# Performance work log

Measured on AMD Instinct MI355X. Metric: run time of the kernel, lower is better.

## Reference

```python
import jax, jax.numpy as jnp
import numpy as np

N, E, R, D = 100000, 1600000, 8, 128

def setup_inputs() -> dict:
    key = jax.random.key(0)
    ks = jax.random.split(key, 8)
    x = jax.random.normal(ks[0], (N, D), dtype=jnp.float32)
    src = jax.random.randint(ks[1], (E,), 0, N, dtype=jnp.int32)
    dst = jax.random.randint(ks[2], (E,), 0, N, dtype=jnp.int32)
    etype = jax.random.randint(ks[3], (E,), 0, R, dtype=jnp.int32)
    W_rel = jax.random.normal(ks[4], (R, D, D), dtype=jnp.float32) * 0.05
    loop_w = jax.random.normal(ks[5], (D, D), dtype=jnp.float32) * 0.05
    rel_bias = jnp.zeros((D,), dtype=jnp.float32)
    W1 = jax.random.normal(ks[6], (2 * D, 2 * D), dtype=jnp.float32) * 0.05
    b1 = jnp.zeros((2 * D,), dtype=jnp.float32)
    W2 = jax.random.normal(ks[7], (3 * D, D), dtype=jnp.float32) * 0.05
    b2 = jnp.zeros((D,), dtype=jnp.float32)
    return {"x": x, "src": src, "dst": dst, "etype": etype,
            "W_rel": W_rel, "loop_w": loop_w, "rel_bias": rel_bias,
            "W1": W1, "b1": b1, "W2": W2, "b2": b2}

def reference(x, src, dst, etype, W_rel, loop_w, rel_bias, W1, b1, W2, b2):
    # RelGraphConv (low_mem): aggregate source features per (relation, dst) node,
    # then one matmul per relation: msg[i] = sum_r (sum_{e: etype=r, dst=i} x[src_e]) @ W_r
    seg = etype.astype(jnp.int32) * N + dst.astype(jnp.int32)  # combined (rel, dst) id
    agg = jax.ops.segment_sum(x[src], seg, num_segments=R * N)  # [R*N, D]
    agg = agg.reshape(R, N, D)
    msg = jnp.einsum('rnd,rdo->no', agg, W_rel)  # per-relation transform + sum over relations
    msg = msg + x @ loop_w + rel_bias            # DGL default self_loop + bias
    # concat-MLP update (activation = tanh)
    mid = jnp.tanh(jnp.concatenate([x, msg], axis=1) @ W1 + b1)  # [N, 2D]
    out = jnp.concatenate([x, mid], axis=1) @ W2 + b2            # [N, D]
    return out
```

## Files before the change

### kernel.cpp

```cpp
#include <hip/hip_runtime.h>

#define NN 100000
#define DD 128
#define RR 8
#define NSEG (RR*NN)
#define NB1 782
#define ECAP 2048

typedef unsigned short u16;
typedef __bf16 bf16x8 __attribute__((ext_vector_type(8)));
typedef float f32x4 __attribute__((ext_vector_type(4)));
typedef u16 ushort4e __attribute__((ext_vector_type(4)));
typedef unsigned int uint4e __attribute__((ext_vector_type(4)));

__device__ __forceinline__ u16 f2bf(float f){
    union { float f; unsigned u; } v; v.f = f;
    unsigned r = v.u + 0x7fffu + ((v.u >> 16) & 1u);
    return (u16)(r >> 16);
}
__device__ __forceinline__ float bf2f(u16 h){
    union { unsigned u; float f; } v; v.u = ((unsigned)h) << 16; return v.f;
}
__device__ __forceinline__ float ftanh(float x){
    float e = __expf(2.0f * x);
    return 1.0f - 2.0f / (e + 1.0f);
}
__device__ __forceinline__ bf16x8 ldv(const u16* p){
    return *reinterpret_cast<const bf16x8*>(p);
}
__device__ __forceinline__ void gload_lds16(const void* g, void* l){
    __builtin_amdgcn_global_load_lds(
        (const __attribute__((address_space(1))) void*)g,
        (__attribute__((address_space(3))) void*)l, 16, 0, 0);
}

__global__ void k_cast_x(const float* __restrict__ x, u16* __restrict__ xb, int n){
    int i = (blockIdx.x * 256 + threadIdx.x) * 4;
    if (i >= n) return;
    float4 v = *reinterpret_cast<const float4*>(x + i);
    ushort4 o = make_ushort4(f2bf(v.x), f2bf(v.y), f2bf(v.z), f2bf(v.w));
    *reinterpret_cast<ushort4*>(xb + i) = o;
}

__global__ void k_prep_w(const float* __restrict__ Wrel, const float* __restrict__ loopw,
                         const float* __restrict__ W1, const float* __restrict__ W2,
                         u16* __restrict__ WT, u16* __restrict__ W1t, u16* __restrict__ W2t){
    int tid = blockIdx.x * 256 + threadIdx.x;
    if (tid < 131072) {
        int r = tid >> 14, rem = tid & 16383, d = rem >> 7, o = rem & 127;
        WT[(r * 128 + o) * 128 + d] = f2bf(Wrel[tid]);
    } else if (tid < 147456) {
        int i = tid - 131072, d = i >> 7, o = i & 127;
        WT[(8 * 128 + o) * 128 + d] = f2bf(loopw[i]);
    } else if (tid < 212992) {
        int i = tid - 147456, k = i >> 8, n2 = i & 255;
        W1t[n2 * 256 + k] = f2bf(W1[i]);
    } else {
        int i = tid - 212992, k = i >> 7, n2 = i & 127;
        W2t[n2 * 384 + k] = f2bf(W2[i]);
    }
}

__global__ void k_count(const int* __restrict__ et, const int* __restrict__ dst,
                        int* __restrict__ cnt, int* __restrict__ seg, int E){
    int e = blockIdx.x * 256 + threadIdx.x;
    if (e < E){
        int s = et[e] * NN + dst[e];
        seg[e] = s;
        atomicAdd(&cnt[s], 1);
    }
}

__global__ void k_scan1(const int* __restrict__ cnt, int* __restrict__ Off, int* __restrict__ bsum){
    __shared__ int lds[256];
    int t = threadIdx.x;
    int i0 = blockIdx.x * 1024 + t * 4;
    int c0 = (i0 + 0 < NSEG) ? cnt[i0 + 0] : 0;
    int c1 = (i0 + 1 < NSEG) ? cnt[i0 + 1] : 0;
    int c2 = (i0 + 2 < NSEG) ? cnt[i0 + 2] : 0;
    int c3 = (i0 + 3 < NSEG) ? cnt[i0 + 3] : 0;
    int s = c0 + c1 + c2 + c3;
    lds[t] = s; __syncthreads();
    for (int off = 1; off < 256; off <<= 1){
        int v = (t >= off) ? lds[t - off] : 0;
        __syncthreads();
        lds[t] += v;
        __syncthreads();
    }
    int excl = lds[t] - s;
    if (i0 + 0 < NSEG) Off[i0 + 0] = excl; excl += c0;
    if (i0 + 1 < NSEG) Off[i0 + 1] = excl; excl += c1;
    if (i0 + 2 < NSEG) Off[i0 + 2] = excl; excl += c2;
    if (i0 + 3 < NSEG) Off[i0 + 3] = excl;
    if (t == 255) bsum[blockIdx.x] = lds[255];
}

__global__ void k_scan2(int* __restrict__ bsum){
    __shared__ int lds[1024];
    int t = threadIdx.x;
    int v = (t < NB1) ? bsum[t] : 0;
    lds[t] = v; __syncthreads();
    for (int off = 1; off < 1024; off <<= 1){
        int u = (t >= off) ? lds[t - off] : 0;
        __syncthreads();
        lds[t] += u;
        __syncthreads();
    }
    if (t < NB1) bsum[t] = lds[t] - v;
}

__global__ void k_scan3(int* __restrict__ Off, const int* __restrict__ bsum,
                        int* __restrict__ cursor, int E){
    int base = bsum[blockIdx.x];
    int t = threadIdx.x;
    int i0 = blockIdx.x * 1024 + t * 4;
    #pragma unroll
    for (int j = 0; j < 4; ++j){
        int i = i0 + j;
        if (i < NSEG){ int v = Off[i] + base; Off[i] = v; cursor[i] = v; }
    }
    if (blockIdx.x == 0 && t == 0) Off[NSEG] = E;
}

__global__ void k_scatter(const int* __restrict__ seg, const int* __restrict__ src,
                          int* __restrict__ cursor, int* __restrict__ esrc, int E){
    int e = blockIdx.x * 256 + threadIdx.x;
    if (e < E){
        int pos = atomicAdd(&cursor[seg[e]], 1);
        esrc[pos] = src[e];
    }
}

__global__ __launch_bounds__(256) void k_agg(
    const u16* __restrict__ xb, const int* __restrict__ Off,
    const int* __restrict__ esrc, u16* __restrict__ agg)
{
    __shared__ int offs[33];
    __shared__ int eidx[ECAP];
    const int tid = threadIdx.x;
    const int s0 = blockIdx.x * 32;
    if (tid < 33) offs[tid] = Off[s0 + tid];
    __syncthreads();
    const int base = offs[0];
    const int tot = offs[32] - base;
    const bool inlds = (tot <= ECAP);
    if (inlds){
        for (int i = tid; i < tot; i += 256) eidx[i] = esrc[base + i];
    }
    __syncthreads();

    const int hw = tid >> 5;
    const int lid = tid & 31;
    const int c = lid * 4;

    #pragma unroll
    for (int j = 0; j < 4; ++j){
        const int sj = hw * 4 + j;
        const int lo = offs[sj] - base;
        const int hi = offs[sj + 1] - base;
        float a0 = 0.f, a1 = 0.f, a2 = 0.f, a3 = 0.f;
        int e = lo;
        if (inlds){
            for (; e + 4 <= hi; e += 4){
                int i0 = eidx[e], i1 = eidx[e+1], i2 = eidx[e+2], i3 = eidx[e+3];
                ushort4 v0 = *reinterpret_cast<const ushort4*>(xb + (size_t)i0 * DD + c);
                ushort4 v1 = *reinterpret_cast<const ushort4*>(xb + (size_t)i1 * DD + c);
                ushort4 v2 = *reinterpret_cast<const ushort4*>(xb + (size_t)i2 * DD + c);
                ushort4 v3 = *reinterpret_cast<const ushort4*>(xb + (size_t)i3 * DD + c);
                a0 += bf2f(v0.x) + bf2f(v1.x) + bf2f(v2.x) + bf2f(v3.x);
                a1 += bf2f(v0.y) + bf2f(v1.y) + bf2f(v2.y) + bf2f(v3.y);
                a2 += bf2f(v0.z) + bf2f(v1.z) + bf2f(v2.z) + bf2f(v3.z);
                a3 += bf2f(v0.w) + bf2f(v1.w) + bf2f(v2.w) + bf2f(v3.w);
            }
            for (; e < hi; ++e){
                int i = eidx[e];
                ushort4 v = *reinterpret_cast<const ushort4*>(xb + (size_t)i * DD + c);
                a0 += bf2f(v.x); a1 += bf2f(v.y); a2 += bf2f(v.z); a3 += bf2f(v.w);
            }
        } else {
            for (; e < hi; ++e){
                int i = esrc[base + e];
                ushort4 v = *reinterpret_cast<const ushort4*>(xb + (size_t)i * DD + c);
                a0 += bf2f(v.x); a1 += bf2f(v.y); a2 += bf2f(v.z); a3 += bf2f(v.w);
            }
        }
        ushort4e o;
        o.x = f2bf(a0); o.y = f2bf(a1); o.z = f2bf(a2); o.w = f2bf(a3);
        __builtin_nontemporal_store(o,
            reinterpret_cast<ushort4e*>(agg + (size_t)(s0 + sj) * DD + c));
    }
}

__global__ __launch_bounds__(512) void k_fused(
    const u16* __restrict__ xb, const u16* __restrict__ agg,
    const u16* __restrict__ WT, const u16* __restrict__ W1t, const u16* __restrict__ W2t,
    const float* __restrict__ relb, const float* __restrict__ bb1, const float* __restrict__ bb2,
    float* __restrict__ out)
{
    __shared__ __align__(16) u16 smem[25088];
    u16 (*bufA)[128] = (u16(*)[128])(smem);
    u16 (*bufB)[128] = (u16(*)[128])(smem + 8192);
    u16 (*msgs)[136] = (u16(*)[136])(smem + 16384);
    u16 (*mids)[264] = (u16(*)[264])(smem + 8192);

    const int tid = threadIdx.x;
    const int w = tid >> 6;
    const int lane = tid & 63;
    const int l15 = lane & 15;
    const int l4 = lane >> 4;
    const int kof = l4 * 8;
    const int swz = (l15 & 7) << 3;
    const int b64 = blockIdx.x * 64;

    const int Wb0 = w * 1024 + (lane << 4);
    auto stage_dma = [&](u16* buf, const u16* grows){
        #pragma unroll
        for (int is = 0; is < 2; ++is){
            int W = Wb0 + is * 8192;
            int row = W >> 8;
            int srcrow = (b64 + row < NN) ? row : 0;
            int inrow = (W & 255) ^ ((row & 7) << 4);
            const char* src = (const char*)(grows + (size_t)srcrow * DD) + inrow;
            gload_lds16(src, (char*)buf + W);
        }
    };

    f32x4 acc[4];
    #pragma unroll
    for (int mi = 0; mi < 4; ++mi)
        #pragma unroll
        for (int q = 0; q < 4; ++q) acc[mi][q] = 0.f;

    stage_dma(&bufA[0][0], agg + (size_t)b64 * DD);
    __syncthreads();

    for (int r = 0; r <= 8; ++r){
        if (r < 7)       stage_dma((r & 1) ? &bufA[0][0] : &bufB[0][0],
                                   agg + ((size_t)(r + 1) * NN + b64) * DD);
        else if (r == 7) stage_dma(&bufA[0][0], xb + (size_t)b64 * DD);
        const u16 (*A)[128] = (r & 1) ? bufB : bufA;
        const u16* B = WT + r * (DD * DD);
        #pragma unroll
        for (int kc = 0; kc < 4; ++kc){
            int cA = (kc * 32 + kof) ^ swz;
            bf16x8 a0 = ldv(&A[l15][cA]);
            bf16x8 a1 = ldv(&A[16 + l15][cA]);
            bf16x8 a2 = ldv(&A[32 + l15][cA]);
            bf16x8 a3 = ldv(&A[48 + l15][cA]);
            bf16x8 wv = ldv(B + (w * 16 + l15) * DD + kc * 32 + kof);
            acc[0] = __builtin_amdgcn_mfma_f32_16x16x32_bf16(a0, wv, acc[0], 0, 0, 0);
            acc[1] = __builtin_amdgcn_mfma_f32_16x16x32_bf16(a1, wv, acc[1], 0, 0, 0);
            acc[2] = __builtin_amdgcn_mfma_f32_16x16x32_bf16(a2, wv, acc[2], 0, 0, 0);
            acc[3] = __builtin_amdgcn_mfma_f32_16x16x32_bf16(a3, wv, acc[3], 0, 0, 0);
        }
        __syncthreads();
    }

    {
        int col = w * 16 + l15;
        float bv = relb[col];
        #pragma unroll
        for (int mi = 0; mi < 4; ++mi)
            #pragma unroll
            for (int q = 0; q < 4; ++q)
                msgs[mi * 16 + l4 * 4 + q][col] = f2bf(acc[mi][q] + bv);
    }
    __syncthreads();

    f32x4 acc2[4][2];
    #pragma unroll
    for (int mi = 0; mi < 4; ++mi)
        #pragma unroll
        for (int nj = 0; nj < 2; ++nj)
            #pragma unroll
            for (int q = 0; q < 4; ++q) acc2[mi][nj][q] = 0.f;

    #pragma unroll
    for (int kc = 0; kc < 8; ++kc){
        bf16x8 a[4];
        #pragma unroll
        for (int mi = 0; mi < 4; ++mi)
            a[mi] = (kc < 4) ? ldv(&bufA[mi * 16 + l15][(kc * 32 + kof) ^ swz])
                             : ldv(&msgs[mi * 16 + l15][(kc - 4) * 32 + kof]);
        #pragma unroll
        for (int nj = 0; nj < 2; ++nj){
            int n2 = w * 32 + nj * 16 + l15;
            bf16x8 wv = ldv(W1t + n2 * 256 + kc * 32 + kof);
            #pragma unroll
            for (int mi = 0; mi < 4; ++mi)
                acc2[mi][nj] = __builtin_amdgcn_mfma_f32_16x16x32_bf16(a[mi], wv, acc2[mi][nj], 0, 0, 0);
        }
    }
    __syncthreads();
    #pragma unroll
    for (int nj = 0; nj < 2; ++nj){
        int col = w * 32 + nj * 16 + l15;
        float bv = bb1[col];
        #pragma unroll
        for (int mi = 0; mi < 4; ++mi)
            #pragma unroll
            for (int q = 0; q < 4; ++q)
                mids[mi * 16 + l4 * 4 + q][col] = f2bf(ftanh(acc2[mi][nj][q] + bv));
    }
    __syncthreads();

    f32x4 acc3[4];
    #pragma unroll
    for (int mi = 0; mi < 4; ++mi)
        #pragma unroll
        for (int q = 0; q < 4; ++q) acc3[mi][q] = 0.f;

    #pragma unroll
    for (int kc = 0; kc < 12; ++kc){
        bf16x8 a[4];
        #pragma unroll
        for (int mi = 0; mi < 4; ++mi)
            a[mi] = (kc < 4) ? ldv(&bufA[mi * 16 + l15][(kc * 32 + kof) ^ swz])
                             : ldv(&mids[mi * 16 + l15][(kc - 4) * 32 + kof]);
        bf16x8 wv = ldv(W2t + (w * 16 + l15) * 384 + kc * 32 + kof);
        #pragma unroll
        for (int mi = 0; mi < 4; ++mi)
            acc3[mi] = __builtin_amdgcn_mfma_f32_16x16x32_bf16(a[mi], wv, acc3[mi], 0, 0, 0);
    }

    {
        int col = w * 16 + l15;
        float bv = bb2[col];
        #pragma unroll
        for (int mi = 0; mi < 4; ++mi)
            #pragma unroll
            for (int q = 0; q < 4; ++q){
                int row = b64 + mi * 16 + l4 * 4 + q;
                if (row < NN)
                    __builtin_nontemporal_store(acc3[mi][q] + bv,
                        &out[(size_t)row * DD + col]);
            }
    }
}

extern "C" void kernel_launch(void* const* d_in, const int* in_sizes, int n_in,
                              void* d_out, int out_size, void* d_ws, size_t ws_size,
                              hipStream_t stream){
    const float* x    = (const float*)d_in[0];
    const int*   src  = (const int*)d_in[1];
    const int*   dst  = (const int*)d_in[2];
    const int*   et   = (const int*)d_in[3];
    const float* Wrel = (const float*)d_in[4];
    const float* loopw= (const float*)d_in[5];
    const float* relb = (const float*)d_in[6];
    const float* W1   = (const float*)d_in[7];
    const float* b1   = (const float*)d_in[8];
    const float* W2   = (const float*)d_in[9];
    const float* b2   = (const float*)d_in[10];
    const int E = in_sizes[1];
    float* out = (float*)d_out;

    char* ws = (char*)d_ws;
    u16* xb   = (u16*)(ws);
    u16* WT   = (u16*)(ws + 25600000);
    u16* W1t  = (u16*)(ws + 25894912);
    u16* W2t  = (u16*)(ws + 26025984);
    int* cnt  = (int*)(ws + 26124288);
    int* Off  = (int*)(ws + 29324288);
    int* bsum = (int*)(ws + 32524544);
    int* esrc = (int*)(ws + 32528640);
    u16* agg  = (u16*)(ws + 38928640);
    int* seg  = (int*)(ws + 38928640);
    if (ws_size < 243728640UL) return;

    hipMemsetAsync(cnt, 0, NSEG * sizeof(int), stream);
    k_cast_x<<<12500, 256, 0, stream>>>(x, xb, NN * DD);
    k_prep_w<<<1024, 256, 0, stream>>>(Wrel, loopw, W1, W2, WT, W1t, W2t);
    k_count<<<(E + 255) / 256, 256, 0, stream>>>(et, dst, cnt, seg, E);
    k_scan1<<<NB1, 256, 0, stream>>>(cnt, Off, bsum);
    k_scan2<<<1, 1024, 0, stream>>>(bsum);
    k_scan3<<<NB1, 256, 0, stream>>>(Off, bsum, cnt, E);
    k_scatter<<<(E + 255) / 256, 256, 0, stream>>>(seg, src, cnt, esrc, E);
    k_agg<<<NSEG / 32, 256, 0, stream>>>(xb, Off, esrc, agg);
    k_fused<<<(NN + 63) / 64, 512, 0, stream>>>(xb, agg, WT, W1t, W2t, relb, b1, b2, out);
}
```

Baseline: 448.6 us.

## Shrink fused-kernel tile to 32 rows and prefetch all relation tiles up front

The fused GEMM kernel now handles 32 rows per block instead of 64. It issues all eight relation agg tiles into LDS at once rather than double-buffering with a sync per relation. The x tile is held in registers and reused for the self-loop and both MLP layers, and the launch bound asks for 4 blocks per CU to raise occupancy. This removes the per-relation barriers and exposes more memory parallelism. The cost is twice as many weight reads from global/L2 per row, and the tail bounds checks are dropped because N divides by 32.

```diff
diff --git a/kernel.cpp b/kernel.cpp
--- a/kernel.cpp
+++ b/kernel.cpp
@@ -191,17 +191,15 @@
     }
 }
 
-__global__ __launch_bounds__(512) void k_fused(
+__global__ __launch_bounds__(512, 4) void k_fused(
     const u16* __restrict__ xb, const u16* __restrict__ agg,
     const u16* __restrict__ WT, const u16* __restrict__ W1t, const u16* __restrict__ W2t,
     const float* __restrict__ relb, const float* __restrict__ bb1, const float* __restrict__ bb2,
     float* __restrict__ out)
 {
-    __shared__ __align__(16) u16 smem[25088];
-    u16 (*bufA)[128] = (u16(*)[128])(smem);
-    u16 (*bufB)[128] = (u16(*)[128])(smem + 8192);
-    u16 (*msgs)[136] = (u16(*)[136])(smem + 16384);
-    u16 (*mids)[264] = (u16(*)[264])(smem + 8192);
+    __shared__ __align__(16) u16 smem[32768];
+    u16 (*msgs)[136] = (u16(*)[136])(smem);
+    u16 (*mids)[264] = (u16(*)[264])(smem + 4352);
 
     const int tid = threadIdx.x;
     const int w = tid >> 6;
@@ -210,66 +208,72 @@
     const int l4 = lane >> 4;
     const int kof = l4 * 8;
     const int swz = (l15 & 7) << 3;
-    const int b64 = blockIdx.x * 64;
-
-    const int Wb0 = w * 1024 + (lane << 4);
-    auto stage_dma = [&](u16* buf, const u16* grows){
-        #pragma unroll
-        for (int is = 0; is < 2; ++is){
-            int W = Wb0 + is * 8192;
-            int row = W >> 8;
-            int srcrow = (b64 + row < NN) ? row : 0;
-            int inrow = (W & 255) ^ ((row & 7) << 4);
-            const char* src = (const char*)(grows + (size_t)srcrow * DD) + inrow;
-            gload_lds16(src, (char*)buf + W);
-        }
-    };
-
-    f32x4 acc[4];
-    #pragma unroll
-    for (int mi = 0; mi < 4; ++mi)
+    const int b32 = blockIdx.x * 32;
+
+    {
+        const int Wb = tid << 4;
+        const int row = Wb >> 8;
+        const int inrow = (Wb & 255) ^ ((row & 7) << 4);
+        #pragma unroll
+        for (int r = 0; r < 8; ++r){
+            const char* src = (const char*)(agg + ((size_t)r * NN + b32 + row) * DD) + inrow;
+            gload_lds16(src, (char*)smem + r * 8192 + Wb);
+        }
+    }
+    bf16x8 xr[2][4];
+    #pragma unroll
+    for (int mi = 0; mi < 2; ++mi)
+        #pragma unroll
+        for (int kc = 0; kc < 4; ++kc)
+            xr[mi][kc] = ldv(xb + (size_t)(b32 + mi * 16 + l15) * DD + kc * 32 + kof);
+
+    __syncthreads();
+
+    f32x4 acc[2];
+    #pragma unroll
+    for (int mi = 0; mi < 2; ++mi)
         #pragma unroll
         for (int q = 0; q < 4; ++q) acc[mi][q] = 0.f;
 
-    stage_dma(&bufA[0][0], agg + (size_t)b64 * DD);
-    __syncthreads();
-
-    for (int r = 0; r <= 8; ++r){
-        if (r < 7)       stage_dma((r & 1) ? &bufA[0][0] : &bufB[0][0],
-                                   agg + ((size_t)(r + 1) * NN + b64) * DD);
-        else if (r == 7) stage_dma(&bufA[0][0], xb + (size_t)b64 * DD);
-        const u16 (*A)[128] = (r & 1) ? bufB : bufA;
+    #pragma unroll
+    for (int r = 0; r < 8; ++r){
+        const u16* T = smem + r * 4096;
         const u16* B = WT + r * (DD * DD);
         #pragma unroll
         for (int kc = 0; kc < 4; ++kc){
             int cA = (kc * 32 + kof) ^ swz;
-            bf16x8 a0 = ldv(&A[l15][cA]);
-            bf16x8 a1 = ldv(&A[16 + l15][cA]);
-            bf16x8 a2 = ldv(&A[32 + l15][cA]);
-            bf16x8 a3 = ldv(&A[48 + l15][cA]);
+            bf16x8 a0 = ldv(T + l15 * 128 + cA);
+            bf16x8 a1 = ldv(T + (16 + l15) * 128 + cA);
             bf16x8 wv = ldv(B + (w * 16 + l15) * DD + kc * 32 + kof);
             acc[0] = __builtin_amdgcn_mfma_f32_16x16x32_bf16(a0, wv, acc[0], 0, 0, 0);
             acc[1] = __builtin_amdgcn_mfma_f32_16x16x32_bf16(a1, wv, acc[1], 0, 0, 0);
-            acc[2] = __builtin_amdgcn_mfma_f32_16x16x32_bf16(a2, wv, acc[2], 0, 0, 0);
-            acc[3] = __builtin_amdgcn_mfma_f32_16x16x32_bf16(a3, wv, acc[3], 0, 0, 0);
-        }
-        __syncthreads();
-    }
+        }
+    }
+    {
+        const u16* B = WT + 8 * (DD * DD);
+        #pragma unroll
+        for (int kc = 0; kc < 4; ++kc){
+            bf16x8 wv = ldv(B + (w * 16 + l15) * DD + kc * 32 + kof);
+            acc[0] = __builtin_amdgcn_mfma_f32_16x16x32_bf16(xr[0][kc], wv, acc[0], 0, 0, 0);
+            acc[1] = __builtin_amdgcn_mfma_f32_16x16x32_bf16(xr[1][kc], wv, acc[1], 0, 0, 0);
+        }
+    }
+    __syncthreads();
 
     {
         int col = w * 16 + l15;
         float bv = relb[col];
         #pragma unroll
-        for (int mi = 0; mi < 4; ++mi)
+        for (int mi = 0; mi < 2; ++mi)
             #pragma unroll
             for (int q = 0; q < 4; ++q)
                 msgs[mi * 16 + l4 * 4 + q][col] = f2bf(acc[mi][q] + bv);
     }
     __syncthreads();
 
-    f32x4 acc2[4][2];
-    #pragma unroll
-    for (int mi = 0; mi < 4; ++mi)
+    f32x4 acc2[2][2];
+    #pragma unroll
+    for (int mi = 0; mi < 2; ++mi)
         #pragma unroll
         for (int nj = 0; nj < 2; ++nj)
             #pragma unroll
@@ -277,63 +281,53 @@
 
     #pragma unroll
     for (int kc = 0; kc < 8; ++kc){
-        bf16x8 a[4];
-        #pragma unroll
-        for (int mi = 0; mi < 4; ++mi)
-            a[mi] = (kc < 4) ? ldv(&bufA[mi * 16 + l15][(kc * 32 + kof) ^ swz])
-                             : ldv(&msgs[mi * 16 + l15][(kc - 4) * 32 + kof]);
+        bf16x8 a0 = (kc < 4) ? xr[0][kc] : ldv(&msgs[l15][(kc - 4) * 32 + kof]);
+        bf16x8 a1 = (kc < 4) ? xr[1][kc] : ldv(&msgs[16 + l15][(kc - 4) * 32 + kof]);
         #pragma unroll
         for (int nj = 0; nj < 2; ++nj){
             int n2 = w * 32 + nj * 16 + l15;
             bf16x8 wv = ldv(W1t + n2 * 256 + kc * 32 + kof);
-            #pragma unroll
-            for (int mi = 0; mi < 4; ++mi)
-                acc2[mi][nj] = __builtin_amdgcn_mfma_f32_16x16x32_bf16(a[mi], wv, acc2[mi][nj], 0, 0, 0);
-        }
-    }
-    __syncthreads();
+            acc2[0][nj] = __builtin_amdgcn_mfma_f32_16x16x32_bf16(a0, wv, acc2[0][nj], 0, 0, 0);
+            acc2[1][nj] = __builtin_amdgcn_mfma_f32_16x16x32_bf16(a1, wv, acc2[1][nj], 0, 0, 0);
+        }
+    }
     #pragma unroll
     for (int nj = 0; nj < 2; ++nj){
         int col = w * 32 + nj * 16 + l15;
         float bv = bb1[col];
         #pragma unroll
-        for (int mi = 0; mi < 4; ++mi)
+        for (int mi = 0; mi < 2; ++mi)
             #pragma unroll
             for (int q = 0; q < 4; ++q)
                 mids[mi * 16 + l4 * 4 + q][col] = f2bf(ftanh(acc2[mi][nj][q] + bv));
     }
     __syncthreads();
 
-    f32x4 acc3[4];
-    #pragma unroll
-    for (int mi = 0; mi < 4; ++mi)
+    f32x4 acc3[2];
+    #pragma unroll
+    for (int mi = 0; mi < 2; ++mi)
         #pragma unroll
         for (int q = 0; q < 4; ++q) acc3[mi][q] = 0.f;
 
     #pragma unroll
     for (int kc = 0; kc < 12; ++kc){
-        bf16x8 a[4];
-        #pragma unroll
-        for (int mi = 0; mi < 4; ++mi)
-            a[mi] = (kc < 4) ? ldv(&bufA[mi * 16 + l15][(kc * 32 + kof) ^ swz])
-                             : ldv(&mids[mi * 16 + l15][(kc - 4) * 32 + kof]);
+        bf16x8 a0 = (kc < 4) ? xr[0][kc] : ldv(&mids[l15][(kc - 4) * 32 + kof]);
+        bf16x8 a1 = (kc < 4) ? xr[1][kc] : ldv(&mids[16 + l15][(kc - 4) * 32 + kof]);
         bf16x8 wv = ldv(W2t + (w * 16 + l15) * 384 + kc * 32 + kof);
-        #pragma unroll
-        for (int mi = 0; mi < 4; ++mi)
-            acc3[mi] = __builtin_amdgcn_mfma_f32_16x16x32_bf16(a[mi], wv, acc3[mi], 0, 0, 0);
+        acc3[0] = __builtin_amdgcn_mfma_f32_16x16x32_bf16(a0, wv, acc3[0], 0, 0, 0);
+        acc3[1] = __builtin_amdgcn_mfma_f32_16x16x32_bf16(a1, wv, acc3[1], 0, 0, 0);
     }
 
     {
         int col = w * 16 + l15;
         float bv = bb2[col];
         #pragma unroll
-        for (int mi = 0; mi < 4; ++mi)
+        for (int mi = 0; mi < 2; ++mi)
             #pragma unroll
             for (int q = 0; q < 4; ++q){
-                int row = b64 + mi * 16 + l4 * 4 + q;
-                if (row < NN)
-                    __builtin_nontemporal_store(acc3[mi][q] + bv,
-                        &out[(size_t)row * DD + col]);
+                int row = b32 + mi * 16 + l4 * 4 + q;
+                __builtin_nontemporal_store(acc3[mi][q] + bv,
+                    &out[(size_t)row * DD + col]);
             }
     }
 }
@@ -377,5 +371,5 @@
     k_scan3<<<NB1, 256, 0, stream>>>(Off, bsum, cnt, E);
     k_scatter<<<(E + 255) / 256, 256, 0, stream>>>(seg, src, cnt, esrc, E);
     k_agg<<<NSEG / 32, 256, 0, stream>>>(xb, Off, esrc, agg);
-    k_fused<<<(NN + 63) / 64, 512, 0, stream>>>(xb, agg, WT, W1t, W2t, relb, b1, b2, out);
-}
+    k_fused<<<NN / 32, 512, 0, stream>>>(xb, agg, WT, W1t, W2t, relb, b1, b2, out);
+}
```

Measured after the change: 534.9 us. +19.2%, slower.

## Transform node features per relation before gathering, bucketing edges by destination only

Applied to the files above, without the earlier changes.

The order of the per-relation matmul and the aggregation is swapped. A new kernel computes y_r = x @ W_r (plus the self-loop) for all nodes. Edges are then bucketed only by destination, storing etype*N+src as the gather index, and a gather kernel sums the transformed rows into msg, adding the self-loop term and bias. This drops the R*N-segment count/scan (8x smaller), the large zero-filled agg buffer and the per-relation matmul loop inside the fused kernel. In exchange it writes a 9xNxD bf16 y tensor, and y is rounded to bf16 before summation, which changes precision. The x cast kernel is removed; bf16 conversion is now done inline with v_cvt_pk_bf16_f32.

```diff
diff --git a/kernel.cpp b/kernel.cpp
--- a/kernel.cpp
+++ b/kernel.cpp
@@ -3,15 +3,12 @@
 #define NN 100000
 #define DD 128
 #define RR 8
-#define NSEG (RR*NN)
-#define NB1 782
+#define NB1 98
 #define ECAP 2048
 
 typedef unsigned short u16;
 typedef __bf16 bf16x8 __attribute__((ext_vector_type(8)));
 typedef float f32x4 __attribute__((ext_vector_type(4)));
-typedef u16 ushort4e __attribute__((ext_vector_type(4)));
-typedef unsigned int uint4e __attribute__((ext_vector_type(4)));
 
 __device__ __forceinline__ u16 f2bf(float f){
     union { float f; unsigned u; } v; v.f = f;
@@ -21,6 +18,17 @@
 __device__ __forceinline__ float bf2f(u16 h){
     union { unsigned u; float f; } v; v.u = ((unsigned)h) << 16; return v.f;
 }
+__device__ __forceinline__ unsigned cvtpk(float lo, float hi){
+    unsigned r;
+    asm("v_cvt_pk_bf16_f32 %0, %1, %2" : "=v"(r) : "v"(lo), "v"(hi));
+    return r;
+}
+__device__ __forceinline__ bf16x8 cvt8(float4 a, float4 b){
+    union { unsigned u[4]; bf16x8 v; } o;
+    o.u[0] = cvtpk(a.x, a.y); o.u[1] = cvtpk(a.z, a.w);
+    o.u[2] = cvtpk(b.x, b.y); o.u[3] = cvtpk(b.z, b.w);
+    return o.v;
+}
 __device__ __forceinline__ float ftanh(float x){
     float e = __expf(2.0f * x);
     return 1.0f - 2.0f / (e + 1.0f);
@@ -32,14 +40,6 @@
     __builtin_amdgcn_global_load_lds(
         (const __attribute__((address_space(1))) void*)g,
         (__attribute__((address_space(3))) void*)l, 16, 0, 0);
-}
-
-__global__ void k_cast_x(const float* __restrict__ x, u16* __restrict__ xb, int n){
-    int i = (blockIdx.x * 256 + threadIdx.x) * 4;
-    if (i >= n) return;
-    float4 v = *reinterpret_cast<const float4*>(x + i);
-    ushort4 o = make_ushort4(f2bf(v.x), f2bf(v.y), f2bf(v.z), f2bf(v.w));
-    *reinterpret_cast<ushort4*>(xb + i) = o;
 }
 
 __global__ void k_prep_w(const float* __restrict__ Wrel, const float* __restrict__ loopw,
@@ -62,12 +62,12 @@
 }
 
 __global__ void k_count(const int* __restrict__ et, const int* __restrict__ dst,
-                        int* __restrict__ cnt, int* __restrict__ seg, int E){
+                        const int* __restrict__ src,
+                        int* __restrict__ cnt, int* __restrict__ gidx, int E){
     int e = blockIdx.x * 256 + threadIdx.x;
     if (e < E){
-        int s = et[e] * NN + dst[e];
-        seg[e] = s;
-        atomicAdd(&cnt[s], 1);
+        gidx[e] = et[e] * NN + src[e];
+        atomicAdd(&cnt[dst[e]], 1);
     }
 }
 
@@ -75,10 +75,10 @@
     __shared__ int lds[256];
     int t = threadIdx.x;
     int i0 = blockIdx.x * 1024 + t * 4;
-    int c0 = (i0 + 0 < NSEG) ? cnt[i0 + 0] : 0;
-    int c1 = (i0 + 1 < NSEG) ? cnt[i0 + 1] : 0;
-    int c2 = (i0 + 2 < NSEG) ? cnt[i0 + 2] : 0;
-    int c3 = (i0 + 3 < NSEG) ? cnt[i0 + 3] : 0;
+    int c0 = (i0 + 0 < NN) ? cnt[i0 + 0] : 0;
+    int c1 = (i0 + 1 < NN) ? cnt[i0 + 1] : 0;
+    int c2 = (i0 + 2 < NN) ? cnt[i0 + 2] : 0;
+    int c3 = (i0 + 3 < NN) ? cnt[i0 + 3] : 0;
     int s = c0 + c1 + c2 + c3;
     lds[t] = s; __syncthreads();
     for (int off = 1; off < 256; off <<= 1){
@@ -88,10 +88,10 @@
         __syncthreads();
     }
     int excl = lds[t] - s;
-    if (i0 + 0 < NSEG) Off[i0 + 0] = excl; excl += c0;
-    if (i0 + 1 < NSEG) Off[i0 + 1] = excl; excl += c1;
-    if (i0 + 2 < NSEG) Off[i0 + 2] = excl; excl += c2;
-    if (i0 + 3 < NSEG) Off[i0 + 3] = excl;
+    if (i0 + 0 < NN) Off[i0 + 0] = excl; excl += c0;
+    if (i0 + 1 < NN) Off[i0 + 1] = excl; excl += c1;
+    if (i0 + 2 < NN) Off[i0 + 2] = excl; excl += c2;
+    if (i0 + 3 < NN) Off[i0 + 3] = excl;
     if (t == 255) bsum[blockIdx.x] = lds[255];
 }
 
@@ -117,23 +117,75 @@
     #pragma unroll
     for (int j = 0; j < 4; ++j){
         int i = i0 + j;
-        if (i < NSEG){ int v = Off[i] + base; Off[i] = v; cursor[i] = v; }
-    }
-    if (blockIdx.x == 0 && t == 0) Off[NSEG] = E;
-}
-
-__global__ void k_scatter(const int* __restrict__ seg, const int* __restrict__ src,
+        if (i < NN){ int v = Off[i] + base; Off[i] = v; cursor[i] = v; }
+    }
+    if (blockIdx.x == 0 && t == 0) Off[NN] = E;
+}
+
+__global__ void k_scatter(const int* __restrict__ dst, const int* __restrict__ gidx,
                           int* __restrict__ cursor, int* __restrict__ esrc, int E){
     int e = blockIdx.x * 256 + threadIdx.x;
     if (e < E){
-        int pos = atomicAdd(&cursor[seg[e]], 1);
-        esrc[pos] = src[e];
-    }
-}
-
-__global__ __launch_bounds__(256) void k_agg(
-    const u16* __restrict__ xb, const int* __restrict__ Off,
-    const int* __restrict__ esrc, u16* __restrict__ agg)
+        int pos = atomicAdd(&cursor[dst[e]], 1);
+        esrc[pos] = gidx[e];
+    }
+}
+
+__global__ __launch_bounds__(512) void k_y(
+    const float* __restrict__ x, const u16* __restrict__ WT, u16* __restrict__ y)
+{
+    const int tid = threadIdx.x;
+    const int w = tid >> 6;
+    const int lane = tid & 63;
+    const int l15 = lane & 15;
+    const int l4 = lane >> 4;
+    const int kof = l4 * 8;
+    const int b64 = blockIdx.x * 64;
+
+    bf16x8 xr[4][4];
+    #pragma unroll
+    for (int mi = 0; mi < 4; ++mi){
+        int rr = b64 + mi * 16 + l15; if (rr >= NN) rr = NN - 1;
+        #pragma unroll
+        for (int kc = 0; kc < 4; ++kc){
+            const float* px = x + (size_t)rr * DD + kc * 32 + kof;
+            xr[mi][kc] = cvt8(*reinterpret_cast<const float4*>(px),
+                              *reinterpret_cast<const float4*>(px + 4));
+        }
+    }
+
+    for (int r = 0; r < 9; ++r){
+        f32x4 acc[4];
+        #pragma unroll
+        for (int mi = 0; mi < 4; ++mi)
+            #pragma unroll
+            for (int q = 0; q < 4; ++q) acc[mi][q] = 0.f;
+        const u16* B = WT + r * (DD * DD);
+        #pragma unroll
+        for (int kc = 0; kc < 4; ++kc){
+            bf16x8 wv = ldv(B + (w * 16 + l15) * DD + kc * 32 + kof);
+            #pragma unroll
+            for (int mi = 0; mi < 4; ++mi)
+                acc[mi] = __builtin_amdgcn_mfma_f32_16x16x32_bf16(xr[mi][kc], wv, acc[mi], 0, 0, 0);
+        }
+        int col = w * 16 + l15;
+        #pragma unroll
+        for (int mi = 0; mi < 4; ++mi){
+            #pragma unroll
+            for (int q = 0; q < 4; q += 2){
+                int row0 = b64 + mi * 16 + l4 * 4 + q;
+                unsigned p = cvtpk(acc[mi][q], acc[mi][q + 1]);
+                if (row0 < NN)     y[((size_t)r * NN + row0) * DD + col] = (u16)(p & 0xffffu);
+                if (row0 + 1 < NN) y[((size_t)r * NN + row0 + 1) * DD + col] = (u16)(p >> 16);
+            }
+        }
+    }
+}
+
+__global__ __launch_bounds__(256) void k_gath(
+    const u16* __restrict__ y, const int* __restrict__ Off,
+    const int* __restrict__ esrc, const float* __restrict__ relb,
+    u16* __restrict__ msg)
 {
     __shared__ int offs[33];
     __shared__ int eidx[ECAP];
@@ -152,21 +204,25 @@
     const int hw = tid >> 5;
     const int lid = tid & 31;
     const int c = lid * 4;
+    const float rb0 = relb[c], rb1 = relb[c+1], rb2 = relb[c+2], rb3 = relb[c+3];
 
     #pragma unroll
     for (int j = 0; j < 4; ++j){
         const int sj = hw * 4 + j;
+        const int node = s0 + sj;
         const int lo = offs[sj] - base;
         const int hi = offs[sj + 1] - base;
-        float a0 = 0.f, a1 = 0.f, a2 = 0.f, a3 = 0.f;
+        ushort4 v8 = *reinterpret_cast<const ushort4*>(y + ((size_t)8 * NN + node) * DD + c);
+        float a0 = bf2f(v8.x) + rb0, a1 = bf2f(v8.y) + rb1;
+        float a2 = bf2f(v8.z) + rb2, a3 = bf2f(v8.w) + rb3;
         int e = lo;
         if (inlds){
             for (; e + 4 <= hi; e += 4){
                 int i0 = eidx[e], i1 = eidx[e+1], i2 = eidx[e+2], i3 = eidx[e+3];
-                ushort4 v0 = *reinterpret_cast<const ushort4*>(xb + (size_t)i0 * DD + c);
-                ushort4 v1 = *reinterpret_cast<const ushort4*>(xb + (size_t)i1 * DD + c);
-                ushort4 v2 = *reinterpret_cast<const ushort4*>(xb + (size_t)i2 * DD + c);
-                ushort4 v3 = *reinterpret_cast<const ushort4*>(xb + (size_t)i3 * DD + c);
+                ushort4 v0 = *reinterpret_cast<const ushort4*>(y + (size_t)i0 * DD + c);
+                ushort4 v1 = *reinterpret_cast<const ushort4*>(y + (size_t)i1 * DD + c);
+                ushort4 v2 = *reinterpret_cast<const ushort4*>(y + (size_t)i2 * DD + c);
+                ushort4 v3 = *reinterpret_cast<const ushort4*>(y + (size_t)i3 * DD + c);
                 a0 += bf2f(v0.x) + bf2f(v1.x) + bf2f(v2.x) + bf2f(v3.x);
                 a1 += bf2f(v0.y) + bf2f(v1.y) + bf2f(v2.y) + bf2f(v3.y);
                 a2 += bf2f(v0.z) + bf2f(v1.z) + bf2f(v2.z) + bf2f(v3.z);
@@ -174,33 +230,29 @@
             }
             for (; e < hi; ++e){
                 int i = eidx[e];
-                ushort4 v = *reinterpret_cast<const ushort4*>(xb + (size_t)i * DD + c);
+                ushort4 v = *reinterpret_cast<const ushort4*>(y + (size_t)i * DD + c);
                 a0 += bf2f(v.x); a1 += bf2f(v.y); a2 += bf2f(v.z); a3 += bf2f(v.w);
             }
         } else {
             for (; e < hi; ++e){
                 int i = esrc[base + e];
-                ushort4 v = *reinterpret_cast<const ushort4*>(xb + (size_t)i * DD + c);
+                ushort4 v = *reinterpret_cast<const ushort4*>(y + (size_t)i * DD + c);
                 a0 += bf2f(v.x); a1 += bf2f(v.y); a2 += bf2f(v.z); a3 += bf2f(v.w);
             }
         }
-        ushort4e o;
-        o.x = f2bf(a0); o.y = f2bf(a1); o.z = f2bf(a2); o.w = f2bf(a3);
-        __builtin_nontemporal_store(o,
-            reinterpret_cast<ushort4e*>(agg + (size_t)(s0 + sj) * DD + c));
-    }
-}
-
-__global__ __launch_bounds__(512) void k_fused(
-    const u16* __restrict__ xb, const u16* __restrict__ agg,
-    const u16* __restrict__ WT, const u16* __restrict__ W1t, const u16* __restrict__ W2t,
-    const float* __restrict__ relb, const float* __restrict__ bb1, const float* __restrict__ bb2,
+        unsigned p0 = cvtpk(a0, a1), p1 = cvtpk(a2, a3);
+        uint2 ov; ov.x = p0; ov.y = p1;
+        *reinterpret_cast<uint2*>(msg + (size_t)node * DD + c) = ov;
+    }
+}
+
+__global__ __launch_bounds__(512, 2) void k_fused(
+    const float* __restrict__ x, const u16* __restrict__ msg,
+    const u16* __restrict__ W1t, const u16* __restrict__ W2t,
+    const float* __restrict__ bb1, const float* __restrict__ bb2,
     float* __restrict__ out)
 {
     __shared__ __align__(16) u16 smem[25088];
-    u16 (*bufA)[128] = (u16(*)[128])(smem);
-    u16 (*bufB)[128] = (u16(*)[128])(smem + 8192);
-    u16 (*msgs)[136] = (u16(*)[136])(smem + 16384);
     u16 (*mids)[264] = (u16(*)[264])(smem + 8192);
 
     const int tid = threadIdx.x;
@@ -212,58 +264,25 @@
     const int swz = (l15 & 7) << 3;
     const int b64 = blockIdx.x * 64;
 
-    const int Wb0 = w * 1024 + (lane << 4);
-    auto stage_dma = [&](u16* buf, const u16* grows){
-        #pragma unroll
-        for (int is = 0; is < 2; ++is){
-            int W = Wb0 + is * 8192;
-            int row = W >> 8;
-            int srcrow = (b64 + row < NN) ? row : 0;
-            int inrow = (W & 255) ^ ((row & 7) << 4);
-            const char* src = (const char*)(grows + (size_t)srcrow * DD) + inrow;
-            gload_lds16(src, (char*)buf + W);
-        }
-    };
-
-    f32x4 acc[4];
-    #pragma unroll
-    for (int mi = 0; mi < 4; ++mi)
-        #pragma unroll
-        for (int q = 0; q < 4; ++q) acc[mi][q] = 0.f;
-
-    stage_dma(&bufA[0][0], agg + (size_t)b64 * DD);
-    __syncthreads();
-
-    for (int r = 0; r <= 8; ++r){
-        if (r < 7)       stage_dma((r & 1) ? &bufA[0][0] : &bufB[0][0],
-                                   agg + ((size_t)(r + 1) * NN + b64) * DD);
-        else if (r == 7) stage_dma(&bufA[0][0], xb + (size_t)b64 * DD);
-        const u16 (*A)[128] = (r & 1) ? bufB : bufA;
-        const u16* B = WT + r * (DD * DD);
+    #pragma unroll
+    for (int is = 0; is < 2; ++is){
+        int W = tid * 16 + is * 8192;
+        int row = W >> 8;
+        int srow = (b64 + row < NN) ? row : 0;
+        int inrow = (W & 255) ^ ((row & 7) << 4);
+        const char* src = (const char*)(msg + (size_t)(b64 + srow) * DD) + inrow;
+        gload_lds16(src, (char*)smem + W);
+    }
+    bf16x8 xr[4][4];
+    #pragma unroll
+    for (int mi = 0; mi < 4; ++mi){
+        int rr = b64 + mi * 16 + l15; if (rr >= NN) rr = NN - 1;
         #pragma unroll
         for (int kc = 0; kc < 4; ++kc){
-            int cA = (kc * 32 + kof) ^ swz;
-            bf16x8 a0 = ldv(&A[l15][cA]);
-            bf16x8 a1 = ldv(&A[16 + l15][cA]);
-            bf16x8 a2 = ldv(&A[32 + l15][cA]);
-            bf16x8 a3 = ldv(&A[48 + l15][cA]);
-            bf16x8 wv = ldv(B + (w * 16 + l15) * DD + kc * 32 + kof);
-            acc[0] = __builtin_amdgcn_mfma_f32_16x16x32_bf16(a0, wv, acc[0], 0, 0, 0);
-            acc[1] = __builtin_amdgcn_mfma_f32_16x16x32_bf16(a1, wv, acc[1], 0, 0, 0);
-            acc[2] = __builtin_amdgcn_mfma_f32_16x16x32_bf16(a2, wv, acc[2], 0, 0, 0);
-            acc[3] = __builtin_amdgcn_mfma_f32_16x16x32_bf16(a3, wv, acc[3], 0, 0, 0);
-        }
-        __syncthreads();
-    }
-
-    {
-        int col = w * 16 + l15;
-        float bv = relb[col];
-        #pragma unroll
-        for (int mi = 0; mi < 4; ++mi)
-            #pragma unroll
-            for (int q = 0; q < 4; ++q)
-                msgs[mi * 16 + l4 * 4 + q][col] = f2bf(acc[mi][q] + bv);
+            const float* px = x + (size_t)rr * DD + kc * 32 + kof;
+            xr[mi][kc] = cvt8(*reinterpret_cast<const float4*>(px),
+                              *reinterpret_cast<const float4*>(px + 4));
+        }
     }
     __syncthreads();
 
@@ -280,8 +299,8 @@
         bf16x8 a[4];
         #pragma unroll
         for (int mi = 0; mi < 4; ++mi)
-            a[mi] = (kc < 4) ? ldv(&bufA[mi * 16 + l15][(kc * 32 + kof) ^ swz])
-                             : ldv(&msgs[mi * 16 + l15][(kc - 4) * 32 + kof]);
+            a[mi] = (kc < 4) ? xr[mi][kc]
+                             : ldv(smem + (mi * 16 + l15) * 128 + (((kc - 4) * 32 + kof) ^ swz));
         #pragma unroll
         for (int nj = 0; nj < 2; ++nj){
             int n2 = w * 32 + nj * 16 + l15;
@@ -291,7 +310,6 @@
                 acc2[mi][nj] = __builtin_amdgcn_mfma_f32_16x16x32_bf16(a[mi], wv, acc2[mi][nj], 0, 0, 0);
         }
     }
-    __syncthreads();
     #pragma unroll
     for (int nj = 0; nj < 2; ++nj){
         int col = w * 32 + nj * 16 + l15;
@@ -315,7 +333,7 @@
         bf16x8 a[4];
         #pragma unroll
         for (int mi = 0; mi < 4; ++mi)
-            a[mi] = (kc < 4) ? ldv(&bufA[mi * 16 + l15][(kc * 32 + kof) ^ swz])
+            a[mi] = (kc < 4) ? xr[mi][kc]
                              : ldv(&mids[mi * 16 + l15][(kc - 4) * 32 + kof]);
         bf16x8 wv = ldv(W2t + (w * 16 + l15) * 384 + kc * 32 + kof);
         #pragma unroll
@@ -356,26 +374,26 @@
     float* out = (float*)d_out;
 
     char* ws = (char*)d_ws;
-    u16* xb   = (u16*)(ws);
-    u16* WT   = (u16*)(ws + 25600000);
-    u16* W1t  = (u16*)(ws + 25894912);
-    u16* W2t  = (u16*)(ws + 26025984);
-    int* cnt  = (int*)(ws + 26124288);
-    int* Off  = (int*)(ws + 29324288);
-    int* bsum = (int*)(ws + 32524544);
-    int* esrc = (int*)(ws + 32528640);
-    u16* agg  = (u16*)(ws + 38928640);
-    int* seg  = (int*)(ws + 38928640);
-    if (ws_size < 243728640UL) return;
-
-    hipMemsetAsync(cnt, 0, NSEG * sizeof(int), stream);
-    k_cast_x<<<12500, 256, 0, stream>>>(x, xb, NN * DD);
+    u16* WT   = (u16*)(ws);
+    u16* W1t  = (u16*)(ws + 294912);
+    u16* W2t  = (u16*)(ws + 425984);
+    int* cnt  = (int*)(ws + 524288);
+    int* Off  = (int*)(ws + 924288);
+    int* bsum = (int*)(ws + 1324416);
+    int* esrc = (int*)(ws + 1328512);
+    u16* y    = (u16*)(ws + 7728512);
+    int* gidx = (int*)(ws + 7728512);
+    u16* msg  = y + (size_t)8 * NN * DD;
+    if (ws_size < 238128512UL) return;
+
+    hipMemsetAsync(cnt, 0, NN * sizeof(int), stream);
     k_prep_w<<<1024, 256, 0, stream>>>(Wrel, loopw, W1, W2, WT, W1t, W2t);
-    k_count<<<(E + 255) / 256, 256, 0, stream>>>(et, dst, cnt, seg, E);
+    k_count<<<(E + 255) / 256, 256, 0, stream>>>(et, dst, src, cnt, gidx, E);
     k_scan1<<<NB1, 256, 0, stream>>>(cnt, Off, bsum);
     k_scan2<<<1, 1024, 0, stream>>>(bsum);
     k_scan3<<<NB1, 256, 0, stream>>>(Off, bsum, cnt, E);
-    k_scatter<<<(E + 255) / 256, 256, 0, stream>>>(seg, src, cnt, esrc, E);
-    k_agg<<<NSEG / 32, 256, 0, stream>>>(xb, Off, esrc, agg);
-    k_fused<<<(NN + 63) / 64, 512, 0, stream>>>(xb, agg, WT, W1t, W2t, relb, b1, b2, out);
-}
+    k_scatter<<<(E + 255) / 256, 256, 0, stream>>>(dst, gidx, cnt, esrc, E);
+    k_y<<<(NN + 63) / 64, 512, 0, stream>>>(x, WT, y);
+    k_gath<<<NN / 32, 256, 0, stream>>>(y, Off, esrc, relb, msg);
+    k_fused<<<(NN + 63) / 64, 512, 0, stream>>>(x, msg, W1t, W2t, b1, b2, out);
+}
```

After: 549.7 us. +22.5%, slower.

## Fuse per-relation gather aggregation into the MLP kernel, dropping the agg buffer

Applied to the files above, without the earlier changes.

The separate aggregation kernel that wrote a bf16 [R*N, D] buffer to global memory is removed. Each fused block now gathers and sums source rows for its 64 destination nodes per relation straight into double-buffered LDS, overlapping the next relation's gather with the current relation's MFMA. The aim is to eliminate the global write and re-read of the large aggregate tensor and one kernel launch. In exchange the gather runs inside a kernel with fewer blocks (1563 of 512 threads), so latency hiding for the random gathers may suffer, and LDS use per block rises to 64KB. It also adds packed bf16 conversion and swizzled layouts for the msgs and mids buffers.

```diff
diff --git a/kernel.cpp b/kernel.cpp
--- a/kernel.cpp
+++ b/kernel.cpp
@@ -5,13 +5,11 @@
 #define RR 8
 #define NSEG (RR*NN)
 #define NB1 782
-#define ECAP 2048
+#define MCAP 3072
 
 typedef unsigned short u16;
 typedef __bf16 bf16x8 __attribute__((ext_vector_type(8)));
 typedef float f32x4 __attribute__((ext_vector_type(4)));
-typedef u16 ushort4e __attribute__((ext_vector_type(4)));
-typedef unsigned int uint4e __attribute__((ext_vector_type(4)));
 
 __device__ __forceinline__ u16 f2bf(float f){
     union { float f; unsigned u; } v; v.f = f;
@@ -20,6 +18,11 @@
 }
 __device__ __forceinline__ float bf2f(u16 h){
     union { unsigned u; float f; } v; v.u = ((unsigned)h) << 16; return v.f;
+}
+__device__ __forceinline__ unsigned cvtpk(float lo, float hi){
+    unsigned r;
+    asm("v_cvt_pk_bf16_f32 %0, %1, %2" : "=v"(r) : "v"(lo), "v"(hi));
+    return r;
 }
 __device__ __forceinline__ float ftanh(float x){
     float e = __expf(2.0f * x);
@@ -131,97 +134,93 @@
     }
 }
 
-__global__ __launch_bounds__(256) void k_agg(
-    const u16* __restrict__ xb, const int* __restrict__ Off,
-    const int* __restrict__ esrc, u16* __restrict__ agg)
-{
-    __shared__ int offs[33];
-    __shared__ int eidx[ECAP];
-    const int tid = threadIdx.x;
-    const int s0 = blockIdx.x * 32;
-    if (tid < 33) offs[tid] = Off[s0 + tid];
-    __syncthreads();
-    const int base = offs[0];
-    const int tot = offs[32] - base;
-    const bool inlds = (tot <= ECAP);
-    if (inlds){
-        for (int i = tid; i < tot; i += 256) eidx[i] = esrc[base + i];
-    }
-    __syncthreads();
-
-    const int hw = tid >> 5;
-    const int lid = tid & 31;
-    const int c = lid * 4;
-
-    #pragma unroll
-    for (int j = 0; j < 4; ++j){
-        const int sj = hw * 4 + j;
-        const int lo = offs[sj] - base;
-        const int hi = offs[sj + 1] - base;
-        float a0 = 0.f, a1 = 0.f, a2 = 0.f, a3 = 0.f;
-        int e = lo;
-        if (inlds){
-            for (; e + 4 <= hi; e += 4){
-                int i0 = eidx[e], i1 = eidx[e+1], i2 = eidx[e+2], i3 = eidx[e+3];
-                ushort4 v0 = *reinterpret_cast<const ushort4*>(xb + (size_t)i0 * DD + c);
-                ushort4 v1 = *reinterpret_cast<const ushort4*>(xb + (size_t)i1 * DD + c);
-                ushort4 v2 = *reinterpret_cast<const ushort4*>(xb + (size_t)i2 * DD + c);
-                ushort4 v3 = *reinterpret_cast<const ushort4*>(xb + (size_t)i3 * DD + c);
-                a0 += bf2f(v0.x) + bf2f(v1.x) + bf2f(v2.x) + bf2f(v3.x);
-                a1 += bf2f(v0.y) + bf2f(v1.y) + bf2f(v2.y) + bf2f(v3.y);
-                a2 += bf2f(v0.z) + bf2f(v1.z) + bf2f(v2.z) + bf2f(v3.z);
-                a3 += bf2f(v0.w) + bf2f(v1.w) + bf2f(v2.w) + bf2f(v3.w);
-            }
-            for (; e < hi; ++e){
-                int i = eidx[e];
-                ushort4 v = *reinterpret_cast<const ushort4*>(xb + (size_t)i * DD + c);
-                a0 += bf2f(v.x); a1 += bf2f(v.y); a2 += bf2f(v.z); a3 += bf2f(v.w);
-            }
-        } else {
-            for (; e < hi; ++e){
-                int i = esrc[base + e];
-                ushort4 v = *reinterpret_cast<const ushort4*>(xb + (size_t)i * DD + c);
-                a0 += bf2f(v.x); a1 += bf2f(v.y); a2 += bf2f(v.z); a3 += bf2f(v.w);
-            }
-        }
-        ushort4e o;
-        o.x = f2bf(a0); o.y = f2bf(a1); o.z = f2bf(a2); o.w = f2bf(a3);
-        __builtin_nontemporal_store(o,
-            reinterpret_cast<ushort4e*>(agg + (size_t)(s0 + sj) * DD + c));
-    }
-}
-
-__global__ __launch_bounds__(512) void k_fused(
-    const u16* __restrict__ xb, const u16* __restrict__ agg,
+__global__ __launch_bounds__(512, 4) void k_mega(
+    const u16* __restrict__ xb, const int* __restrict__ Off, const int* __restrict__ esrc,
     const u16* __restrict__ WT, const u16* __restrict__ W1t, const u16* __restrict__ W2t,
     const float* __restrict__ relb, const float* __restrict__ bb1, const float* __restrict__ bb2,
     float* __restrict__ out)
 {
-    __shared__ __align__(16) u16 smem[25088];
-    u16 (*bufA)[128] = (u16(*)[128])(smem);
-    u16 (*bufB)[128] = (u16(*)[128])(smem + 8192);
-    u16 (*msgs)[136] = (u16(*)[136])(smem + 16384);
-    u16 (*mids)[264] = (u16(*)[264])(smem + 8192);
+    __shared__ __align__(16) u16 smem[32768];
+    u16* xt    = smem;
+    int* offs  = (int*)((char*)smem + 16384);
+    int* ebase = (int*)((char*)smem + 18464);
+    int* eidx  = (int*)((char*)smem + 18560);
+    u16* agg0  = (u16*)((char*)smem + 31104);
+    u16* agg1  = (u16*)((char*)smem + 47488);
+    u16* msgs  = (u16*)((char*)smem + 16384);
+    u16* mids  = (u16*)((char*)smem + 32768);
 
     const int tid = threadIdx.x;
-    const int w = tid >> 6;
-    const int lane = tid & 63;
-    const int l15 = lane & 15;
-    const int l4 = lane >> 4;
+    const int w = tid >> 6, lane = tid & 63, l15 = lane & 15, l4 = lane >> 4;
     const int kof = l4 * 8;
     const int swz = (l15 & 7) << 3;
     const int b64 = blockIdx.x * 64;
-
-    const int Wb0 = w * 1024 + (lane << 4);
-    auto stage_dma = [&](u16* buf, const u16* grows){
-        #pragma unroll
-        for (int is = 0; is < 2; ++is){
-            int W = Wb0 + is * 8192;
-            int row = W >> 8;
-            int srcrow = (b64 + row < NN) ? row : 0;
-            int inrow = (W & 255) ^ ((row & 7) << 4);
-            const char* src = (const char*)(grows + (size_t)srcrow * DD) + inrow;
-            gload_lds16(src, (char*)buf + W);
+    const int hw = tid >> 5, lid = tid & 31, c = lid * 4;
+
+    #pragma unroll
+    for (int is = 0; is < 2; ++is){
+        int W = tid * 16 + is * 8192;
+        int row = W >> 8;
+        int srow = (b64 + row < NN) ? row : 0;
+        int inrow = (W & 255) ^ ((row & 7) << 4);
+        gload_lds16((const char*)(xb + (size_t)(b64 + srow) * DD) + inrow, (char*)smem + W);
+    }
+    for (int i = tid; i < 520; i += 512){
+        int r = i / 65, j = i - r * 65;
+        int node = b64 + j; if (node > NN) node = NN;
+        offs[i] = Off[r * NN + node];
+    }
+    __syncthreads();
+    if (tid == 0){
+        int b = 0;
+        #pragma unroll
+        for (int r = 0; r < 8; ++r){ ebase[r] = b; b += offs[r * 65 + 64] - offs[r * 65]; }
+        ebase[8] = b;
+    }
+    __syncthreads();
+    const int tot = ebase[8];
+    const bool inlds = (tot <= MCAP);
+    if (inlds){
+        for (int r = 0; r < 8; ++r){
+            int o0 = offs[r * 65], n = offs[r * 65 + 64] - o0, eb = ebase[r];
+            for (int i = tid; i < n; i += 512) eidx[eb + i] = esrc[o0 + i];
+        }
+    }
+    __syncthreads();
+
+    auto gather = [&](u16* buf, int r){
+        const int o0 = offs[r * 65];
+        const int eb = ebase[r] - o0;
+        #pragma unroll
+        for (int j = 0; j < 4; ++j){
+            const int sj = hw * 4 + j;
+            const int lo = offs[r * 65 + sj], hi = offs[r * 65 + sj + 1];
+            const int n = hi - lo;
+            float a0 = 0.f, a1 = 0.f, a2 = 0.f, a3 = 0.f;
+            if (inlds){
+                const int base = eb + lo;
+                #pragma unroll
+                for (int k = 0; k < 4; ++k){
+                    if (k < n){
+                        int id = eidx[base + k];
+                        ushort4 v = *reinterpret_cast<const ushort4*>(xb + (size_t)id * DD + c);
+                        a0 += bf2f(v.x); a1 += bf2f(v.y); a2 += bf2f(v.z); a3 += bf2f(v.w);
+                    }
+                }
+                for (int k = 4; k < n; ++k){
+                    int id = eidx[base + k];
+                    ushort4 v = *reinterpret_cast<const ushort4*>(xb + (size_t)id * DD + c);
+                    a0 += bf2f(v.x); a1 += bf2f(v.y); a2 += bf2f(v.z); a3 += bf2f(v.w);
+                }
+            } else {
+                for (int e = lo; e < hi; ++e){
+                    int id = esrc[e];
+                    ushort4 v = *reinterpret_cast<const ushort4*>(xb + (size_t)id * DD + c);
+                    a0 += bf2f(v.x); a1 += bf2f(v.y); a2 += bf2f(v.z); a3 += bf2f(v.w);
+                }
+            }
+            uint2 p; p.x = cvtpk(a0, a1); p.y = cvtpk(a2, a3);
+            *reinterpret_cast<uint2*>(buf + sj * 128 + (c ^ ((sj & 7) << 3))) = p;
         }
     };
 
@@ -231,22 +230,20 @@
         #pragma unroll
         for (int q = 0; q < 4; ++q) acc[mi][q] = 0.f;
 
-    stage_dma(&bufA[0][0], agg + (size_t)b64 * DD);
-    __syncthreads();
-
-    for (int r = 0; r <= 8; ++r){
-        if (r < 7)       stage_dma((r & 1) ? &bufA[0][0] : &bufB[0][0],
-                                   agg + ((size_t)(r + 1) * NN + b64) * DD);
-        else if (r == 7) stage_dma(&bufA[0][0], xb + (size_t)b64 * DD);
-        const u16 (*A)[128] = (r & 1) ? bufB : bufA;
+    gather(agg0, 0);
+    __syncthreads();
+
+    for (int r = 0; r < 8; ++r){
+        if (r < 7) gather((r & 1) ? agg0 : agg1, r + 1);
+        const u16* A = (r & 1) ? agg1 : agg0;
         const u16* B = WT + r * (DD * DD);
         #pragma unroll
         for (int kc = 0; kc < 4; ++kc){
             int cA = (kc * 32 + kof) ^ swz;
-            bf16x8 a0 = ldv(&A[l15][cA]);
-            bf16x8 a1 = ldv(&A[16 + l15][cA]);
-            bf16x8 a2 = ldv(&A[32 + l15][cA]);
-            bf16x8 a3 = ldv(&A[48 + l15][cA]);
+            bf16x8 a0 = ldv(A + (l15) * 128 + cA);
+            bf16x8 a1 = ldv(A + (16 + l15) * 128 + cA);
+            bf16x8 a2 = ldv(A + (32 + l15) * 128 + cA);
+            bf16x8 a3 = ldv(A + (48 + l15) * 128 + cA);
             bf16x8 wv = ldv(B + (w * 16 + l15) * DD + kc * 32 + kof);
             acc[0] = __builtin_amdgcn_mfma_f32_16x16x32_bf16(a0, wv, acc[0], 0, 0, 0);
             acc[1] = __builtin_amdgcn_mfma_f32_16x16x32_bf16(a1, wv, acc[1], 0, 0, 0);
@@ -255,6 +252,22 @@
         }
         __syncthreads();
     }
+    {
+        const u16* B = WT + 8 * (DD * DD);
+        #pragma unroll
+        for (int kc = 0; kc < 4; ++kc){
+            int cA = (kc * 32 + kof) ^ swz;
+            bf16x8 a0 = ldv(xt + (l15) * 128 + cA);
+            bf16x8 a1 = ldv(xt + (16 + l15) * 128 + cA);
+            bf16x8 a2 = ldv(xt + (32 + l15) * 128 + cA);
+            bf16x8 a3 = ldv(xt + (48 + l15) * 128 + cA);
+            bf16x8 wv = ldv(B + (w * 16 + l15) * DD + kc * 32 + kof);
+            acc[0] = __builtin_amdgcn_mfma_f32_16x16x32_bf16(a0, wv, acc[0], 0, 0, 0);
+            acc[1] = __builtin_amdgcn_mfma_f32_16x16x32_bf16(a1, wv, acc[1], 0, 0, 0);
+            acc[2] = __builtin_amdgcn_mfma_f32_16x16x32_bf16(a2, wv, acc[2], 0, 0, 0);
+            acc[3] = __builtin_amdgcn_mfma_f32_16x16x32_bf16(a3, wv, acc[3], 0, 0, 0);
+        }
+    }
 
     {
         int col = w * 16 + l15;
@@ -262,8 +275,10 @@
         #pragma unroll
         for (int mi = 0; mi < 4; ++mi)
             #pragma unroll
-            for (int q = 0; q < 4; ++q)
-                msgs[mi * 16 + l4 * 4 + q][col] = f2bf(acc[mi][q] + bv);
+            for (int q = 0; q < 4; ++q){
+                int row = mi * 16 + l4 * 4 + q;
+                msgs[row * 128 + (col ^ ((row & 7) << 3))] = f2bf(acc[mi][q] + bv);
+            }
     }
     __syncthreads();
 
@@ -279,9 +294,11 @@
     for (int kc = 0; kc < 8; ++kc){
         bf16x8 a[4];
         #pragma unroll
-        for (int mi = 0; mi < 4; ++mi)
-            a[mi] = (kc < 4) ? ldv(&bufA[mi * 16 + l15][(kc * 32 + kof) ^ swz])
-                             : ldv(&msgs[mi * 16 + l15][(kc - 4) * 32 + kof]);
+        for (int mi = 0; mi < 4; ++mi){
+            int cA = ((kc & 3) * 32 + kof) ^ swz;
+            a[mi] = (kc < 4) ? ldv(xt + (mi * 16 + l15) * 128 + cA)
+                             : ldv(msgs + (mi * 16 + l15) * 128 + cA);
+        }
         #pragma unroll
         for (int nj = 0; nj < 2; ++nj){
             int n2 = w * 32 + nj * 16 + l15;
@@ -291,7 +308,6 @@
                 acc2[mi][nj] = __builtin_amdgcn_mfma_f32_16x16x32_bf16(a[mi], wv, acc2[mi][nj], 0, 0, 0);
         }
     }
-    __syncthreads();
     #pragma unroll
     for (int nj = 0; nj < 2; ++nj){
         int col = w * 32 + nj * 16 + l15;
@@ -299,8 +315,10 @@
         #pragma unroll
         for (int mi = 0; mi < 4; ++mi)
             #pragma unroll
-            for (int q = 0; q < 4; ++q)
-                mids[mi * 16 + l4 * 4 + q][col] = f2bf(ftanh(acc2[mi][nj][q] + bv));
+            for (int q = 0; q < 4; ++q){
+                int row = mi * 16 + l4 * 4 + q;
+                mids[row * 256 + (col ^ ((row & 7) << 3))] = f2bf(ftanh(acc2[mi][nj][q] + bv));
+            }
     }
     __syncthreads();
 
@@ -314,9 +332,15 @@
     for (int kc = 0; kc < 12; ++kc){
         bf16x8 a[4];
         #pragma unroll
-        for (int mi = 0; mi < 4; ++mi)
-            a[mi] = (kc < 4) ? ldv(&bufA[mi * 16 + l15][(kc * 32 + kof) ^ swz])
-                             : ldv(&mids[mi * 16 + l15][(kc - 4) * 32 + kof]);
+        for (int mi = 0; mi < 4; ++mi){
+            if (kc < 4){
+                int cA = (kc * 32 + kof) ^ swz;
+                a[mi] = ldv(xt + (mi * 16 + l15) * 128 + cA);
+            } else {
+                int cA = (((kc - 4) * 32) + kof) ^ swz;
+                a[mi] = ldv(mids + (mi * 16 + l15) * 256 + cA);
+            }
+        }
         bf16x8 wv = ldv(W2t + (w * 16 + l15) * 384 + kc * 32 + kof);
         #pragma unroll
         for (int mi = 0; mi < 4; ++mi)
@@ -364,9 +388,8 @@
     int* Off  = (int*)(ws + 29324288);
     int* bsum = (int*)(ws + 32524544);
     int* esrc = (int*)(ws + 32528640);
-    u16* agg  = (u16*)(ws + 38928640);
     int* seg  = (int*)(ws + 38928640);
-    if (ws_size < 243728640UL) return;
+    if (ws_size < 45328640UL) return;
 
     hipMemsetAsync(cnt, 0, NSEG * sizeof(int), stream);
     k_cast_x<<<12500, 256, 0, stream>>>(x, xb, NN * DD);
@@ -376,6 +399,5 @@
     k_scan2<<<1, 1024, 0, stream>>>(bsum);
     k_scan3<<<NB1, 256, 0, stream>>>(Off, bsum, cnt, E);
     k_scatter<<<(E + 255) / 256, 256, 0, stream>>>(seg, src, cnt, esrc, E);
-    k_agg<<<NSEG / 32, 256, 0, stream>>>(xb, Off, esrc, agg);
-    k_fused<<<(NN + 63) / 64, 512, 0, stream>>>(xb, agg, WT, W1t, W2t, relb, b1, b2, out);
-}
+    k_mega<<<(NN + 63) / 64, 512, 0, stream>>>(xb, Off, esrc, WT, W1t, W2t, relb, b1, b2, out);
+}
```

After: 504.8 us. 1.13x slower.
